# Performance work log

Hardware: AMD Instinct MI355X
Metric: run time of the kernel (lower is better)

## Reference

```python
import jax, jax.numpy as jnp
import numpy as np

_EPS = 1e-06


def setup_inputs() -> dict:
    key = jax.random.key(0)
    k1, k2, k3, k4, k5 = jax.random.split(key, 5)
    B, N = 2, 8192
    return {
        "kp_before": jax.random.normal(k1, (B, N, 3), dtype=jnp.float32),
        "kp_warped_pred": jax.random.normal(k2, (B, N, 3), dtype=jnp.float32),
        "pose_gt": jax.random.normal(k3, (B, 3, 4), dtype=jnp.float32),
        "overlap_weights": jax.random.uniform(k4, (B, N), dtype=jnp.float32),
        "inlier_logits": jax.random.normal(k5, (B, N), dtype=jnp.float32),
    }


def _bce_with_logits(x, z):
    # elementwise BCEWithLogits: z*softplus(-x) + (1-z)*softplus(x)
    return z * jax.nn.softplus(-x) + (1.0 - z) * jax.nn.softplus(x)


def _balanced_loss(logits, label):
    # BalancedLoss: mean BCE within each of the 2 label groups, averaged over groups
    bce = _bce_with_logits(logits, label)
    loss = jnp.float32(0.0)
    for i in range(2):
        mask = (label == i).astype(jnp.float32)
        cnt = jnp.sum(mask)
        group = jnp.where(cnt > 0, jnp.sum(bce * mask) / jnp.maximum(cnt, 1.0), 0.0)
        loss = loss + group / 2.0
    return loss


def reference(kp_before, kp_warped_pred, pose_gt, overlap_weights, inlier_logits):
    B, N, _ = kp_before.shape
    M = B * N
    # se3_transform_list: warped_gt[b] = kp_before[b] @ R[b]^T + t[b]
    R = pose_gt[:, :, :3]            # [B,3,3]
    t = pose_gt[:, :, 3]             # [B,3]
    kp_warped_gt = jnp.einsum('bij,bnj->bni', R, kp_before) + t[:, None, :]
    # torch.cat(list, dim=0) over equal-sized chunks == reshape
    pred = kp_warped_pred.reshape(M, 3)
    gt = kp_warped_gt.reshape(M, 3)
    corr_err = pred - gt               # [M,3]
    # pairwise L2 distance matrix [M,M] (O(N^2) traffic) + 1-NN argmin
    sq = (jnp.sum(pred * pred, axis=1)[:, None]
          + jnp.sum(gt * gt, axis=1)[None, :]
          - 2.0 * (pred @ gt.T))
    dist_map = jnp.sqrt(jnp.maximum(sq, 0.0))
    knn_ind = jnp.argmin(dist_map, axis=1)
    binary_mask = (knn_ind == jnp.arange(M)).astype(jnp.float32)
    inlier_err = _balanced_loss(inlier_logits.reshape(M), binary_mask)
    # metric == 'mae'
    err = jnp.sum(jnp.abs(corr_err), axis=-1)  # [M]
    w = overlap_weights.reshape(M)
    mean_err = jnp.sum(w * err) / jnp.maximum(jnp.sum(w), _EPS)
    return mean_err + inlier_err
```

## Files before the change

kernel.cpp:

```cpp
#include <hip/hip_runtime.h>
#include <cstdint>

#define TPB 256
#define PRE_PB 128
#define ROWS_PB 64
#define RBATCH 16

__global__ void __launch_bounds__(TPB) prep_prefix(
        const float* __restrict__ kp_before,
        const float* __restrict__ pred,
        const float* __restrict__ pose,
        float4* __restrict__ gt4,
        float* __restrict__ thr,
        unsigned int* __restrict__ good,
        float* __restrict__ accum,
        int M, int N) {
    __shared__ float4 shg[2 * PRE_PB];
    int tid = threadIdx.x;
    if (blockIdx.x == 0 && tid < 8) accum[tid] = 0.0f;

    int row = blockIdx.x * ROWS_PB + (tid >> 2);
    int sub = tid & 3;
    bool rowvalid = (row < M);
    int i = rowvalid ? row : (M - 1);

    float sp, tp0, tp1, tp2, dii;
    float g0, g1, g2, sg;
    {
        int b = i / N;
        const float* P = pose + b * 12;
        float k0 = kp_before[3*i+0];
        float k1 = kp_before[3*i+1];
        float k2 = kp_before[3*i+2];
        g0 = fmaf(P[2],  k2, fmaf(P[1], k1, P[0]*k0)) + P[3];
        g1 = fmaf(P[6],  k2, fmaf(P[5], k1, P[4]*k0)) + P[7];
        g2 = fmaf(P[10], k2, fmaf(P[9], k1, P[8]*k0)) + P[11];
        {
            #pragma clang fp contract(off)
            sg = (g0*g0 + g1*g1) + g2*g2;
        }
        float p0 = pred[3*i+0], p1 = pred[3*i+1], p2 = pred[3*i+2];
        {
            #pragma clang fp contract(off)
            sp = (p0*p0 + p1*p1) + p2*p2;
        }
        tp0 = 2.0f*p0; tp1 = 2.0f*p1; tp2 = 2.0f*p2;
        float dot2 = fmaf(tp2, g2, fmaf(tp1, g1, tp0*g0));
        float v = (sp + sg) - dot2;
        dii = fmaxf(v, 0.0f);
    }
    if (sub == 0 && rowvalid) {
        gt4[i] = make_float4(g0, g1, g2, sg);
        thr[i] = dii;
    }

    {
        int k = tid;
        int jp = (k < PRE_PB) ? k : (N + k - PRE_PB);
        if (jp >= M) jp = k - PRE_PB;
        const float* Pj = pose + (jp / N) * 12;
        float q0 = kp_before[3*jp+0];
        float q1 = kp_before[3*jp+1];
        float q2 = kp_before[3*jp+2];
        float h0 = fmaf(Pj[2],  q2, fmaf(Pj[1], q1, Pj[0]*q0)) + Pj[3];
        float h1 = fmaf(Pj[6],  q2, fmaf(Pj[5], q1, Pj[4]*q0)) + Pj[7];
        float h2 = fmaf(Pj[10], q2, fmaf(Pj[9], q1, Pj[8]*q0)) + Pj[11];
        float hh;
        {
            #pragma clang fp contract(off)
            hh = (h0*h0 + h1*h1) + h2*h2;
        }
        shg[(k & 63) * 4 + (k >> 6)] = make_float4(h0, h1, h2, hh);
    }
    __syncthreads();

    bool dirty = (i < PRE_PB) || (i >= N && i < N + PRE_PB);
    bool bad;
    if (!dirty) {
        float mn = __uint_as_float(0x7f7fffffu);
        #pragma unroll 8
        for (int it = 0; it < 64; it++) {
            float4 g = shg[it * 4 + sub];
            float v = (sp + g.w) -
                      fmaf(tp2, g.z, fmaf(tp1, g.y, tp0 * g.x));
            mn = fminf(mn, v);
        }
        float v1 = fminf(mn, __shfl_xor(mn, 1, 64));
        float v2 = __shfl_xor(v1, 2, 64);
        if (i >= N + PRE_PB) {
            float mall = fminf(v1, v2);
            bad = (fmaxf(mall, 0.0f) <= dii);
        } else {
            bad = (fmaxf(v1, 0.0f) <= dii) || (fmaxf(v2, 0.0f) < dii);
        }
    } else {
        bool h = false;
        #pragma unroll 8
        for (int it = 0; it < 64; it++) {
            int k = sub * 64 + it;
            int j = (k < PRE_PB) ? k : (N + k - PRE_PB);
            if (j >= M) j = k - PRE_PB;
            float4 g = shg[it * 4 + sub];
            float v = (sp + g.w) -
                      fmaf(tp2, g.z, fmaf(tp1, g.y, tp0 * g.x));
            float c = fmaxf(v, 0.0f);
            h = h || (c < dii && j != i) || (c == dii && j < i);
        }
        int hv = h ? 1 : 0;
        hv |= __shfl_xor(hv, 1, 64);
        hv |= __shfl_xor(hv, 2, 64);
        bad = (hv != 0);
    }
    if (sub == 0 && rowvalid) good[i] = bad ? 0u : 1u;
}

__device__ inline float wave_red(float v) {
    #pragma unroll
    for (int off = 32; off > 0; off >>= 1) v += __shfl_down(v, off, 64);
    return v;
}

__global__ void __launch_bounds__(TPB) resolve_finalize(
        const float* __restrict__ pred,
        const float4* __restrict__ gt4,
        const float* __restrict__ thr,
        const unsigned int* __restrict__ good,
        const float* __restrict__ ow,
        const float* __restrict__ logits,
        float* __restrict__ accum,
        float* __restrict__ out,
        int M, int N) {
    __shared__ unsigned char verd[ROWS_PB];
    __shared__ int cands[ROWS_PB];
    __shared__ int ncand;
    int tid = threadIdx.x;
    int r0 = blockIdx.x * ROWS_PB;

    if (tid == 0) ncand = 0;
    __syncthreads();
    if (tid < ROWS_PB) {
        int i = r0 + tid;
        unsigned int gi = (i < M) ? good[i] : 0u;
        verd[tid] = (unsigned char)gi;
        if (gi) { int p = atomicAdd(&ncand, 1); cands[p] = tid; }
    }
    __syncthreads();
    int nc = ncand;

    for (int e = 0; e < nc; e++) {
        int r = r0 + cands[e];
        float p0 = pred[3*r+0], p1 = pred[3*r+1], p2 = pred[3*r+2];
        float sp;
        {
            #pragma clang fp contract(off)
            sp = (p0*p0 + p1*p1) + p2*p2;
        }
        float tp0 = 2.0f*p0, tp1 = 2.0f*p1, tp2 = 2.0f*p2;
        float dii = thr[r];
        bool h = false;
        #pragma unroll
        for (int half = 0; half < 2; half++) {
            int base = (half == 0) ? PRE_PB : (N + PRE_PB);
            int end  = (half == 0) ? N : M;
            for (int j0 = base + tid; j0 < end; j0 += TPB * RBATCH) {
                float4 g[RBATCH];
                #pragma unroll
                for (int b = 0; b < RBATCH; b++) {
                    int j = j0 + b * TPB;
                    g[b] = gt4[(j < end) ? j : base];
                }
                #pragma unroll
                for (int b = 0; b < RBATCH; b++) {
                    int j = j0 + b * TPB;
                    float v = (sp + g[b].w) -
                              fmaf(tp2, g[b].z, fmaf(tp1, g[b].y, tp0 * g[b].x));
                    float c = fmaxf(v, 0.0f);
                    h = h || ((j < end) &&
                              ((c < dii && j != r) || (c == dii && j < r)));
                }
            }
        }
        if (h) verd[cands[e]] = 0;
    }
    __syncthreads();

    float werr = 0.f, wsum = 0.f, b1 = 0.f, c1 = 0.f, b0 = 0.f, c0 = 0.f;
    if (tid < ROWS_PB && (r0 + tid) < M) {
        int i = r0 + tid;
        float x = logits[i];
        float l1p = log1pf(expf(-fabsf(x)));
        if (verd[tid]) {
            b1 = fmaxf(-x, 0.f) + l1p; c1 = 1.f;
        } else {
            b0 = fmaxf(x, 0.f) + l1p;  c0 = 1.f;
        }
        float4 g = gt4[i];
        float q0 = pred[3*i+0], q1 = pred[3*i+1], q2 = pred[3*i+2];
        float e2 = (fabsf(q0 - g.x) + fabsf(q1 - g.y)) + fabsf(q2 - g.z);
        float wi = ow[i];
        werr = wi * e2;
        wsum = wi;
    }
    werr = wave_red(werr); wsum = wave_red(wsum);
    b1 = wave_red(b1); c1 = wave_red(c1);
    b0 = wave_red(b0); c0 = wave_red(c0);
    if (tid == 0) {
        atomicAdd(&accum[0], werr);
        atomicAdd(&accum[1], wsum);
        atomicAdd(&accum[2], b1);
        atomicAdd(&accum[3], c1);
        atomicAdd(&accum[4], b0);
        atomicAdd(&accum[5], c0);
    }
    __threadfence();
    __syncthreads();
    if (tid == 0) {
        unsigned int* ctr = (unsigned int*)&accum[7];
        unsigned int old = atomicAdd(ctr, 1u);
        if (old == gridDim.x - 1) {
            float a0 = atomicAdd(&accum[0], 0.f);
            float a1 = atomicAdd(&accum[1], 0.f);
            float a2 = atomicAdd(&accum[2], 0.f);
            float a3 = atomicAdd(&accum[3], 0.f);
            float a4 = atomicAdd(&accum[4], 0.f);
            float a5 = atomicAdd(&accum[5], 0.f);
            float mean_err = a0 / fmaxf(a1, 1e-6f);
            float g1v = (a3 > 0.f) ? (a2 / fmaxf(a3, 1.f)) : 0.f;
            float g0v = (a5 > 0.f) ? (a4 / fmaxf(a5, 1.f)) : 0.f;
            out[0] = mean_err + (g0v * 0.5f + g1v * 0.5f);
        }
    }
}

extern "C" void kernel_launch(void* const* d_in, const int* in_sizes, int n_in,
                              void* d_out, int out_size, void* d_ws, size_t ws_size,
                              hipStream_t stream) {
    const float* kp_before = (const float*)d_in[0];
    const float* pred      = (const float*)d_in[1];
    const float* pose      = (const float*)d_in[2];
    const float* ow        = (const float*)d_in[3];
    const float* logits    = (const float*)d_in[4];
    float* out = (float*)d_out;

    int M = in_sizes[3];
    int B = in_sizes[2] / 12;
    int N = M / B;

    char* ws = (char*)d_ws;
    float4* gt4 = (float4*)ws;
    float* thr = (float*)(ws + (size_t)M * 16);
    unsigned int* good = (unsigned int*)(ws + (size_t)M * 20);
    float* accum = (float*)(ws + (size_t)M * 24);

    int nblk = (M + ROWS_PB - 1) / ROWS_PB;

    hipLaunchKernelGGL(prep_prefix, dim3(nblk), dim3(TPB), 0, stream,
                       kp_before, pred, pose, gt4, thr, good, accum, M, N);

    hipLaunchKernelGGL(resolve_finalize, dim3(nblk), dim3(TPB), 0, stream,
                       pred, gt4, thr, good, ow, logits, accum, out, M, N);
}
```

Measured before the change: 107.7 us.

## Split candidate column scan across slice blocks with per-range last-block finalize

The resolve kernel now gives each block 256 candidate rows and one of 16 column slices, instead of having each block scan every column for its 64 rows. A block that finds a closer column for a row clears that row's flag in global memory. A per-range atomic counter lets the last slice block of each range compute the loss terms for that range. The goal is to spread the serial per-candidate scan across many more blocks and cut the loop latency per candidate. In exchange it adds global atomics and cross-block synchronisation. Each thread now covers at most two columns per half, so a slice larger than 512 columns (N above 8320) would leave columns unchecked.

```diff
diff --git a/kernel.cpp b/kernel.cpp
--- a/kernel.cpp
+++ b/kernel.cpp
@@ -4,7 +4,8 @@
 #define TPB 256
 #define PRE_PB 128
 #define ROWS_PB 64
-#define RBATCH 16
+#define RNG 256
+#define NSLICE 16
 
 __global__ void __launch_bounds__(TPB) prep_prefix(
         const float* __restrict__ kp_before,
@@ -14,10 +15,14 @@
         float* __restrict__ thr,
         unsigned int* __restrict__ good,
         float* __restrict__ accum,
-        int M, int N) {
+        unsigned int* __restrict__ rctr,
+        int M, int N, int nranges) {
     __shared__ float4 shg[2 * PRE_PB];
     int tid = threadIdx.x;
-    if (blockIdx.x == 0 && tid < 8) accum[tid] = 0.0f;
+    if (blockIdx.x == 0) {
+        if (tid < 8) accum[tid] = 0.0f;
+        for (int k = tid; k < nranges; k += TPB) rctr[k] = 0u;
+    }
 
     int row = blockIdx.x * ROWS_PB + (tid >> 2);
     int sub = tid & 3;
@@ -124,31 +129,40 @@
         const float* __restrict__ pred,
         const float4* __restrict__ gt4,
         const float* __restrict__ thr,
-        const unsigned int* __restrict__ good,
+        unsigned int* __restrict__ good,
         const float* __restrict__ ow,
         const float* __restrict__ logits,
         float* __restrict__ accum,
+        unsigned int* __restrict__ rctr,
         float* __restrict__ out,
-        int M, int N) {
-    __shared__ unsigned char verd[ROWS_PB];
-    __shared__ int cands[ROWS_PB];
+        int M, int N, int nranges) {
+    __shared__ int cands[RNG];
     __shared__ int ncand;
+    __shared__ int lastflag;
     int tid = threadIdx.x;
-    int r0 = blockIdx.x * ROWS_PB;
+    int rg = blockIdx.x >> 4;
+    int s  = blockIdx.x & (NSLICE - 1);
+    int r0 = rg * RNG;
 
     if (tid == 0) ncand = 0;
     __syncthreads();
-    if (tid < ROWS_PB) {
-        int i = r0 + tid;
-        unsigned int gi = (i < M) ? good[i] : 0u;
-        verd[tid] = (unsigned char)gi;
-        if (gi) { int p = atomicAdd(&ncand, 1); cands[p] = tid; }
-    }
+    int i = r0 + tid;
+    unsigned int gi = (i < M) ? good[i] : 0u;
+    if (gi == 1u) { int p = atomicAdd(&ncand, 1); cands[p] = i; }
     __syncthreads();
     int nc = ncand;
 
+    int C0 = N - PRE_PB;
+    int per0 = (C0 + NSLICE - 1) / NSLICE;
+    int js0 = PRE_PB + s * per0;
+    int je0 = js0 + per0; if (je0 > N) je0 = N;
+    int C1 = (M - N) - PRE_PB; if (C1 < 0) C1 = 0;
+    int per1 = (C1 + NSLICE - 1) / NSLICE;
+    int js1 = N + PRE_PB + s * per1;
+    int je1 = js1 + per1; if (je1 > M) je1 = M;
+
     for (int e = 0; e < nc; e++) {
-        int r = r0 + cands[e];
+        int r = cands[e];
         float p0 = pred[3*r+0], p1 = pred[3*r+1], p2 = pred[3*r+2];
         float sp;
         {
@@ -157,39 +171,59 @@
         }
         float tp0 = 2.0f*p0, tp1 = 2.0f*p1, tp2 = 2.0f*p2;
         float dii = thr[r];
+
+        int ja0 = js0 + tid;        bool va0 = (ja0 < je0);
+        int jb0 = ja0 + TPB;        bool vb0 = (jb0 < je0);
+        int ja1 = js1 + tid;        bool va1 = (C1 > 0) && (ja1 < je1);
+        int jb1 = ja1 + TPB;        bool vb1 = (C1 > 0) && (jb1 < je1);
+        float4 gA0 = gt4[va0 ? ja0 : PRE_PB];
+        float4 gB0 = gt4[vb0 ? jb0 : PRE_PB];
+        float4 gA1 = gt4[va1 ? ja1 : PRE_PB];
+        float4 gB1 = gt4[vb1 ? jb1 : PRE_PB];
+
         bool h = false;
-        #pragma unroll
-        for (int half = 0; half < 2; half++) {
-            int base = (half == 0) ? PRE_PB : (N + PRE_PB);
-            int end  = (half == 0) ? N : M;
-            for (int j0 = base + tid; j0 < end; j0 += TPB * RBATCH) {
-                float4 g[RBATCH];
-                #pragma unroll
-                for (int b = 0; b < RBATCH; b++) {
-                    int j = j0 + b * TPB;
-                    g[b] = gt4[(j < end) ? j : base];
-                }
-                #pragma unroll
-                for (int b = 0; b < RBATCH; b++) {
-                    int j = j0 + b * TPB;
-                    float v = (sp + g[b].w) -
-                              fmaf(tp2, g[b].z, fmaf(tp1, g[b].y, tp0 * g[b].x));
-                    float c = fmaxf(v, 0.0f);
-                    h = h || ((j < end) &&
-                              ((c < dii && j != r) || (c == dii && j < r)));
-                }
-            }
-        }
-        if (h) verd[cands[e]] = 0;
-    }
-    __syncthreads();
+        {
+            float v = (sp + gA0.w) -
+                      fmaf(tp2, gA0.z, fmaf(tp1, gA0.y, tp0 * gA0.x));
+            float c = fmaxf(v, 0.0f);
+            h = h || (va0 && ((c < dii && ja0 != r) || (c == dii && ja0 < r)));
+        }
+        {
+            float v = (sp + gB0.w) -
+                      fmaf(tp2, gB0.z, fmaf(tp1, gB0.y, tp0 * gB0.x));
+            float c = fmaxf(v, 0.0f);
+            h = h || (vb0 && ((c < dii && jb0 != r) || (c == dii && jb0 < r)));
+        }
+        {
+            float v = (sp + gA1.w) -
+                      fmaf(tp2, gA1.z, fmaf(tp1, gA1.y, tp0 * gA1.x));
+            float c = fmaxf(v, 0.0f);
+            h = h || (va1 && ((c < dii && ja1 != r) || (c == dii && ja1 < r)));
+        }
+        {
+            float v = (sp + gB1.w) -
+                      fmaf(tp2, gB1.z, fmaf(tp1, gB1.y, tp0 * gB1.x));
+            float c = fmaxf(v, 0.0f);
+            h = h || (vb1 && ((c < dii && jb1 != r) || (c == dii && jb1 < r)));
+        }
+        if (h) good[r] = 0u;
+    }
+
+    __threadfence();
+    __syncthreads();
+    if (tid == 0) {
+        unsigned int old = atomicAdd(&rctr[rg], 1u);
+        lastflag = (old == NSLICE - 1) ? 1 : 0;
+    }
+    __syncthreads();
+    if (!lastflag) return;
 
     float werr = 0.f, wsum = 0.f, b1 = 0.f, c1 = 0.f, b0 = 0.f, c0 = 0.f;
-    if (tid < ROWS_PB && (r0 + tid) < M) {
-        int i = r0 + tid;
+    if (i < M) {
+        unsigned int gfin = atomicOr(&good[i], 0u);
         float x = logits[i];
         float l1p = log1pf(expf(-fabsf(x)));
-        if (verd[tid]) {
+        if (gfin == 1u) {
             b1 = fmaxf(-x, 0.f) + l1p; c1 = 1.f;
         } else {
             b0 = fmaxf(x, 0.f) + l1p;  c0 = 1.f;
@@ -204,7 +238,7 @@
     werr = wave_red(werr); wsum = wave_red(wsum);
     b1 = wave_red(b1); c1 = wave_red(c1);
     b0 = wave_red(b0); c0 = wave_red(c0);
-    if (tid == 0) {
+    if ((tid & 63) == 0) {
         atomicAdd(&accum[0], werr);
         atomicAdd(&accum[1], wsum);
         atomicAdd(&accum[2], b1);
@@ -217,7 +251,7 @@
     if (tid == 0) {
         unsigned int* ctr = (unsigned int*)&accum[7];
         unsigned int old = atomicAdd(ctr, 1u);
-        if (old == gridDim.x - 1) {
+        if (old == (unsigned int)(nranges - 1)) {
             float a0 = atomicAdd(&accum[0], 0.f);
             float a1 = atomicAdd(&accum[1], 0.f);
             float a2 = atomicAdd(&accum[2], 0.f);
@@ -251,12 +285,16 @@
     float* thr = (float*)(ws + (size_t)M * 16);
     unsigned int* good = (unsigned int*)(ws + (size_t)M * 20);
     float* accum = (float*)(ws + (size_t)M * 24);
-
-    int nblk = (M + ROWS_PB - 1) / ROWS_PB;
-
-    hipLaunchKernelGGL(prep_prefix, dim3(nblk), dim3(TPB), 0, stream,
-                       kp_before, pred, pose, gt4, thr, good, accum, M, N);
-
-    hipLaunchKernelGGL(resolve_finalize, dim3(nblk), dim3(TPB), 0, stream,
-                       pred, gt4, thr, good, ow, logits, accum, out, M, N);
+    unsigned int* rctr = (unsigned int*)(ws + (size_t)M * 24 + 32);
+
+    int nranges = (M + RNG - 1) / RNG;
+    int nblk1 = (M + ROWS_PB - 1) / ROWS_PB;
+
+    hipLaunchKernelGGL(prep_prefix, dim3(nblk1), dim3(TPB), 0, stream,
+                       kp_before, pred, pose, gt4, thr, good, accum, rctr,
+                       M, N, nranges);
+
+    hipLaunchKernelGGL(resolve_finalize, dim3(nranges * NSLICE), dim3(TPB), 0,
+                       stream, pred, gt4, thr, good, ow, logits, accum, rctr,
+                       out, M, N, nranges);
 }
```

After: 156.8 us. 45.6% more time.
